# Optimization experiments

Hardware: AMD Instinct MI355X
Metric: run time of the kernel (lower is better)

## Reference

```python
import jax, jax.numpy as jnp
import numpy as np

EPS = 1e-6

def setup_inputs() -> dict:
    key = jax.random.key(0)
    ks = jax.random.split(key, 6)
    N, E, Din, H, D = 50000, 800000, 256, 4, 32
    x = jax.random.normal(ks[0], (N, Din), dtype=jnp.float32)
    adj_indices = jax.random.randint(ks[1], (E, 2), 0, N, dtype=jnp.int32)
    adj_weights = jax.random.uniform(ks[2], (E,), dtype=jnp.float32)
    W = jax.random.normal(ks[3], (Din, H * D), dtype=jnp.float32) * (1.0 / np.sqrt(Din))
    a_src = jax.random.normal(ks[4], (H, D), dtype=jnp.float32)
    a_dst = jax.random.normal(ks[5], (H, D), dtype=jnp.float32)
    return {"x": x, "adj_indices": adj_indices, "adj_weights": adj_weights,
            "W": W, "a_src": a_src, "a_dst": a_dst}

def reference(x, adj_indices, adj_weights, W, a_src, a_dst):
    N = x.shape[0]
    H, D = a_src.shape
    h = (x @ W).reshape(N, H, D)                       # [N,H,D]
    src = adj_indices[:, 0]
    dst = adj_indices[:, 1]
    hs = h[src]                                        # [E,H,D]
    hd = h[dst]                                        # [E,H,D]
    raw = jnp.einsum('ehd,hd->eh', hs, a_src) + jnp.einsum('ehd,hd->eh', hd, a_dst)
    gate = jnp.clip(adj_weights, EPS, None)[:, None]   # [E,1]
    scores = jnp.tanh(raw) + jnp.log(gate)             # [E,H]
    # per-destination segment softmax (numerically stable)
    seg_max = jax.ops.segment_max(scores, dst, num_segments=N)   # [N,H]
    ex = jnp.exp(scores - seg_max[dst])
    denom = jax.ops.segment_sum(ex, dst, num_segments=N)         # [N,H]
    alpha = ex / denom[dst]                            # softmax over edges per dst
    alpha = alpha * gate
    messages = alpha[:, :, None] * hs                  # [E,H,D]
    out = jax.ops.segment_sum(messages, dst, num_segments=N)     # [N,H,D]
    out = out.reshape(N, H * D)
    return jax.nn.gelu(out, approximate=False)
```

## Files before the change

kernel.cpp:

```cpp
#include <hip/hip_runtime.h>
#include <hip/hip_bf16.h>

#define N_NODES 50000
#define N_EDGES 800000
#define DIN 256
#define HD 128
#define NH 4
#define CAP 64
#define CSTR 16

#define GROWS 64
#define LDKH 136

#define GEMM_BLOCKS ((N_NODES + GROWS - 1) / GROWS)
#define SCAT_BLOCKS ((N_EDGES + 255) / 256)

typedef __bf16 bf16x8 __attribute__((ext_vector_type(8)));
typedef float  f32x4  __attribute__((ext_vector_type(4)));

static __device__ __forceinline__ unsigned short f2bu(float v) {
  union { __hip_bfloat16 b; unsigned short u; } c;
  c.b = __float2bfloat16(v);
  return c.u;
}

static __device__ __forceinline__ unsigned short f2hu(float v) {
  union { _Float16 h; unsigned short u; } c;
  c.h = (_Float16)v;
  return c.u;
}

static __device__ __forceinline__ float hu2f(unsigned short u) {
  union { _Float16 h; unsigned short u; } c;
  c.u = u;
  return (float)c.h;
}

__global__ void init_kernel(const float* __restrict__ W,
                            unsigned short* __restrict__ WtF,
                            int* __restrict__ cursor) {
  int i = blockIdx.x * 256 + threadIdx.x;
  if (i < HD * DIN) {
    int j    = i & 7;
    int lane = (i >> 3) & 63;
    int t    = (i >> 9) & 7;
    int s    = (i >> 12) & 3;
    int ks   = (i >> 14) & 1;
    int m = lane & 15, q = lane >> 4;
    int k = ks * 128 + 32 * s + 8 * q + j;
    int c = 16 * t + m;
    WtF[i] = f2bu(W[k * HD + c]);
  }
  if (i < N_NODES * CSTR) cursor[i] = 0;
}

__global__ __launch_bounds__(256, 2) void gemm_kernel(
    const float* __restrict__ x,
    const unsigned short* __restrict__ WtF,
    const float* __restrict__ a_src,
    const float* __restrict__ a_dst,
    unsigned short* __restrict__ hbf,
    float* __restrict__ ssrc,
    float* __restrict__ sdst) {
  __shared__ unsigned short xs[GROWS * LDKH];
  const int tid = threadIdx.x;

  const int row0 = blockIdx.x * GROWS;
  const int wid  = tid >> 6;
  const int lane = tid & 63;
  const int m    = lane & 15;
  const int q    = lane >> 4;

  float4 v0[8];
#pragma unroll
  for (int it = 0; it < 8; it++) {
    int i = it * 256 + tid, r = i >> 5, kq = i & 31;
    int row = row0 + r;
    v0[it] = (row < N_NODES) ? *(const float4*)(x + (size_t)row * DIN + 4 * kq)
                             : make_float4(0.f, 0.f, 0.f, 0.f);
  }
#pragma unroll
  for (int it = 0; it < 8; it++) {
    int i = it * 256 + tid, r = i >> 5, kq = i & 31;
    ushort4 b;
    b.x = f2bu(v0[it].x); b.y = f2bu(v0[it].y); b.z = f2bu(v0[it].z); b.w = f2bu(v0[it].w);
    *(ushort4*)&xs[r * LDKH + 4 * kq] = b;
  }
  __syncthreads();

  f32x4 acc[8];
#pragma unroll
  for (int t = 0; t < 8; t++) acc[t] = (f32x4){0.f, 0.f, 0.f, 0.f};

  const unsigned short* xbase = &xs[(wid * 16 + m) * LDKH];

  bf16x8 a0[4];
#pragma unroll
  for (int s = 0; s < 4; s++) a0[s] = *(const bf16x8*)(xbase + 32 * s + 8 * q);

  float4 v1[8];
#pragma unroll
  for (int it = 0; it < 8; it++) {
    int i = it * 256 + tid, r = i >> 5, kq = i & 31;
    int row = row0 + r;
    v1[it] = (row < N_NODES) ? *(const float4*)(x + (size_t)row * DIN + 128 + 4 * kq)
                             : make_float4(0.f, 0.f, 0.f, 0.f);
  }

#pragma unroll
  for (int s = 0; s < 4; s++) {
    bf16x8 bfr[8];
#pragma unroll
    for (int t = 0; t < 8; t++)
      bfr[t] = *(const bf16x8*)(WtF + (size_t)((0 * 4 + s) * 8 + t) * 512 + lane * 8);
#pragma unroll
    for (int t = 0; t < 8; t++)
      acc[t] = __builtin_amdgcn_mfma_f32_16x16x32_bf16(a0[s], bfr[t], acc[t], 0, 0, 0);
  }
  __syncthreads();

#pragma unroll
  for (int it = 0; it < 8; it++) {
    int i = it * 256 + tid, r = i >> 5, kq = i & 31;
    ushort4 b;
    b.x = f2bu(v1[it].x); b.y = f2bu(v1[it].y); b.z = f2bu(v1[it].z); b.w = f2bu(v1[it].w);
    *(ushort4*)&xs[r * LDKH + 4 * kq] = b;
  }
  __syncthreads();

  bf16x8 a1[4];
#pragma unroll
  for (int s = 0; s < 4; s++) a1[s] = *(const bf16x8*)(xbase + 32 * s + 8 * q);

#pragma unroll
  for (int s = 0; s < 4; s++) {
    bf16x8 bfr[8];
#pragma unroll
    for (int t = 0; t < 8; t++)
      bfr[t] = *(const bf16x8*)(WtF + (size_t)((1 * 4 + s) * 8 + t) * 512 + lane * 8);
#pragma unroll
    for (int t = 0; t < 8; t++)
      acc[t] = __builtin_amdgcn_mfma_f32_16x16x32_bf16(a1[s], bfr[t], acc[t], 0, 0, 0);
  }

#pragma unroll
  for (int t = 0; t < 8; t++) {
#pragma unroll
    for (int r = 0; r < 4; r++) {
      int row = row0 + wid * 16 + q * 4 + r;
      if (row < N_NODES) hbf[(size_t)row * HD + 16 * t + m] = f2bu(acc[t][r]);
    }
  }

  float as[8], ad[8];
#pragma unroll
  for (int t = 0; t < 8; t++) {
    as[t] = a_src[16 * t + m];
    ad[t] = a_dst[16 * t + m];
  }
#pragma unroll
  for (int r = 0; r < 4; r++) {
    float ps[NH] = {0.f, 0.f, 0.f, 0.f};
    float pd[NH] = {0.f, 0.f, 0.f, 0.f};
#pragma unroll
    for (int t = 0; t < 8; t++) {
      ps[t >> 1] = fmaf(acc[t][r], as[t], ps[t >> 1]);
      pd[t >> 1] = fmaf(acc[t][r], ad[t], pd[t >> 1]);
    }
#pragma unroll
    for (int mm = 8; mm >= 1; mm >>= 1) {
#pragma unroll
      for (int hh = 0; hh < NH; hh++) {
        ps[hh] += __shfl_xor(ps[hh], mm, 64);
        pd[hh] += __shfl_xor(pd[hh], mm, 64);
      }
    }
    int row = row0 + wid * 16 + q * 4 + r;
    if (m == 0 && row < N_NODES) {
#pragma unroll
      for (int hh = 0; hh < NH; hh++) {
        ssrc[row * NH + hh] = ps[hh];
        sdst[row * NH + hh] = pd[hh];
      }
    }
  }
}

__global__ __launch_bounds__(256, 4) void scatter_kernel(
    const int2* __restrict__ adj,
    const float* __restrict__ wts,
    int* __restrict__ cursor,
    unsigned int* __restrict__ slots) {
  int e = blockIdx.x * 256 + threadIdx.x;
  if (e >= N_EDGES) return;
  int2 sd = adj[e];
  if ((unsigned)sd.x >= (unsigned)N_NODES || (unsigned)sd.y >= (unsigned)N_NODES) return;
  float g = fmaxf(wts[e], 1e-6f);
  int pos = atomicAdd(&cursor[sd.y * CSTR], 1);
  if (pos >= CAP) pos = CAP - 1;
  unsigned packed = ((unsigned)f2hu(g) << 16) | (unsigned)(sd.x & 0xffff);
  __builtin_nontemporal_store(packed, &slots[((size_t)sd.y << 6) + pos]);
}

__global__ __launch_bounds__(128, 4) void node_kernel(
    const int* __restrict__ cursor,
    const unsigned int* __restrict__ slots,
    const float4* __restrict__ ssrc4,
    const float4* __restrict__ sdst4,
    const unsigned int* __restrict__ hbf32,
    float* __restrict__ out) {
  const int tid  = threadIdx.x;
  const int wid  = tid >> 6;
  const int lane = tid & 63;
  const int n    = blockIdx.x * 2 + wid;
  const int hh   = lane >> 4;

  int deg = cursor[n * CSTR];
  if (deg > CAP) deg = CAP;

  __shared__ int    sidx[2][CAP];
  __shared__ float4 swv[2][CAP];

  float4 ex = make_float4(0.f, 0.f, 0.f, 0.f);
  if (lane < deg) {
    unsigned sl = slots[((size_t)n << 6) + lane];
    int s = (int)(sl & 0xffffu);
    float g = hu2f((unsigned short)(sl >> 16));
    float4 ss = ssrc4[s];
    float4 sd = sdst4[n];
    ex.x = g * expf(tanhf(ss.x + sd.x));
    ex.y = g * expf(tanhf(ss.y + sd.y));
    ex.z = g * expf(tanhf(ss.z + sd.z));
    ex.w = g * expf(tanhf(ss.w + sd.w));
    sidx[wid][lane] = s;
    swv[wid][lane] = make_float4(ex.x * g, ex.y * g, ex.z * g, ex.w * g);
  }

  float4 tot = ex;
#pragma unroll
  for (int mm = 32; mm >= 1; mm >>= 1) {
    tot.x += __shfl_xor(tot.x, mm, 64);
    tot.y += __shfl_xor(tot.y, mm, 64);
    tot.z += __shfl_xor(tot.z, mm, 64);
    tot.w += __shfl_xor(tot.w, mm, 64);
  }
  float dn  = (hh == 0) ? tot.x : (hh == 1) ? tot.y : (hh == 2) ? tot.z : tot.w;
  float inv = (dn > 0.f) ? 1.f / dn : 0.f;
  __syncthreads();

  float acc0 = 0.f, acc1 = 0.f;
  int j = 0;
  for (; j + 8 <= deg; j += 8) {
    int s0 = sidx[wid][j + 0], s1 = sidx[wid][j + 1];
    int s2 = sidx[wid][j + 2], s3 = sidx[wid][j + 3];
    int s4 = sidx[wid][j + 4], s5 = sidx[wid][j + 5];
    int s6 = sidx[wid][j + 6], s7 = sidx[wid][j + 7];
    unsigned u0 = hbf32[(size_t)s0 * (HD / 2) + lane];
    unsigned u1 = hbf32[(size_t)s1 * (HD / 2) + lane];
    unsigned u2 = hbf32[(size_t)s2 * (HD / 2) + lane];
    unsigned u3 = hbf32[(size_t)s3 * (HD / 2) + lane];
    unsigned u4 = hbf32[(size_t)s4 * (HD / 2) + lane];
    unsigned u5 = hbf32[(size_t)s5 * (HD / 2) + lane];
    unsigned u6 = hbf32[(size_t)s6 * (HD / 2) + lane];
    unsigned u7 = hbf32[(size_t)s7 * (HD / 2) + lane];
    float w0 = ((const float*)&swv[wid][j + 0])[hh];
    float w1 = ((const float*)&swv[wid][j + 1])[hh];
    float w2 = ((const float*)&swv[wid][j + 2])[hh];
    float w3 = ((const float*)&swv[wid][j + 3])[hh];
    float w4 = ((const float*)&swv[wid][j + 4])[hh];
    float w5 = ((const float*)&swv[wid][j + 5])[hh];
    float w6 = ((const float*)&swv[wid][j + 6])[hh];
    float w7 = ((const float*)&swv[wid][j + 7])[hh];
    acc0 = fmaf(w0, __uint_as_float(u0 << 16), acc0);
    acc1 = fmaf(w0, __uint_as_float(u0 & 0xffff0000u), acc1);
    acc0 = fmaf(w1, __uint_as_float(u1 << 16), acc0);
    acc1 = fmaf(w1, __uint_as_float(u1 & 0xffff0000u), acc1);
    acc0 = fmaf(w2, __uint_as_float(u2 << 16), acc0);
    acc1 = fmaf(w2, __uint_as_float(u2 & 0xffff0000u), acc1);
    acc0 = fmaf(w3, __uint_as_float(u3 << 16), acc0);
    acc1 = fmaf(w3, __uint_as_float(u3 & 0xffff0000u), acc1);
    acc0 = fmaf(w4, __uint_as_float(u4 << 16), acc0);
    acc1 = fmaf(w4, __uint_as_float(u4 & 0xffff0000u), acc1);
    acc0 = fmaf(w5, __uint_as_float(u5 << 16), acc0);
    acc1 = fmaf(w5, __uint_as_float(u5 & 0xffff0000u), acc1);
    acc0 = fmaf(w6, __uint_as_float(u6 << 16), acc0);
    acc1 = fmaf(w6, __uint_as_float(u6 & 0xffff0000u), acc1);
    acc0 = fmaf(w7, __uint_as_float(u7 << 16), acc0);
    acc1 = fmaf(w7, __uint_as_float(u7 & 0xffff0000u), acc1);
  }
  for (; j < deg; j++) {
    int s0 = sidx[wid][j];
    unsigned u0 = hbf32[(size_t)s0 * (HD / 2) + lane];
    float w0 = ((const float*)&swv[wid][j])[hh];
    acc0 = fmaf(w0, __uint_as_float(u0 << 16), acc0);
    acc1 = fmaf(w0, __uint_as_float(u0 & 0xffff0000u), acc1);
  }
  acc0 *= inv;
  acc1 *= inv;

  float2 gl;
  gl.x = 0.5f * acc0 * (1.f + erff(acc0 * 0.70710678118654752f));
  gl.y = 0.5f * acc1 * (1.f + erff(acc1 * 0.70710678118654752f));
  *(float2*)&out[(size_t)n * HD + 2 * lane] = gl;
}

extern "C" void kernel_launch(void* const* d_in, const int* in_sizes, int n_in,
                              void* d_out, int out_size, void* d_ws, size_t ws_size,
                              hipStream_t stream) {
  const float* x     = (const float*)d_in[0];
  const int2*  adj   = (const int2*)d_in[1];
  const float* wts   = (const float*)d_in[2];
  const float* W     = (const float*)d_in[3];
  const float* a_src = (const float*)d_in[4];
  const float* a_dst = (const float*)d_in[5];
  float* out = (float*)d_out;

  char* p = (char*)d_ws;
  auto carve = [&](size_t bytes) {
    char* q = p;
    p += (bytes + 255) & ~(size_t)255;
    return (void*)q;
  };
  unsigned short* hbf = (unsigned short*)carve((size_t)N_NODES * HD * sizeof(unsigned short));
  unsigned short* WtF = (unsigned short*)carve((size_t)HD * DIN * sizeof(unsigned short));
  float* ssrc   = (float*)carve((size_t)N_NODES * NH * sizeof(float));
  float* sdst   = (float*)carve((size_t)N_NODES * NH * sizeof(float));
  unsigned int* slots = (unsigned int*)carve((size_t)N_NODES * CAP * sizeof(unsigned int));
  int*   cursor = (int*)carve((size_t)N_NODES * CSTR * sizeof(int));

  init_kernel<<<(N_NODES * CSTR + 255) / 256, 256, 0, stream>>>(W, WtF, cursor);
  scatter_kernel<<<SCAT_BLOCKS, 256, 0, stream>>>(adj, wts, cursor, slots);
  gemm_kernel<<<GEMM_BLOCKS, 256, 0, stream>>>(x, WtF, a_src, a_dst, hbf, ssrc, sdst);
  node_kernel<<<N_NODES / 2, 128, 0, stream>>>(cursor, slots, (const float4*)ssrc,
                                               (const float4*)sdst,
                                               (const unsigned int*)hbf, out);
}
```

Measured before the change: 221.3 us.

## Shard per-destination edge buckets by block to reduce atomic contention

Replaces the single padded per-node cursor (stride 16) and 64-slot bucket with 8 shards selected by block index. Each shard has its own dense cursor array and 16-slot buckets. The node kernel gathers the shard counts, compacts the slots into shared memory, and then runs as before. Cursor zeroing moves to hipMemsetAsync so init_kernel only converts W. The change targets atomic contention and the padded cursor footprint, at the cost of more cursor and slot reads per node plus an extra barrier. Per-shard overflow is clamped at 16, whereas the old limit was 64 for the whole node.

```diff
diff --git a/kernel.cpp b/kernel.cpp
--- a/kernel.cpp
+++ b/kernel.cpp
@@ -7,7 +7,8 @@
 #define HD 128
 #define NH 4
 #define CAP 64
-#define CSTR 16
+#define NSH 8
+#define SCAP 16
 
 #define GROWS 64
 #define LDKH 136
@@ -37,8 +38,7 @@
 }
 
 __global__ void init_kernel(const float* __restrict__ W,
-                            unsigned short* __restrict__ WtF,
-                            int* __restrict__ cursor) {
+                            unsigned short* __restrict__ WtF) {
   int i = blockIdx.x * 256 + threadIdx.x;
   if (i < HD * DIN) {
     int j    = i & 7;
@@ -51,7 +51,23 @@
     int c = 16 * t + m;
     WtF[i] = f2bu(W[k * HD + c]);
   }
-  if (i < N_NODES * CSTR) cursor[i] = 0;
+}
+
+__global__ __launch_bounds__(256, 4) void scatter_kernel(
+    const int2* __restrict__ adj,
+    const float* __restrict__ wts,
+    int* __restrict__ cursor_s,
+    unsigned int* __restrict__ slots_s) {
+  int e = blockIdx.x * 256 + threadIdx.x;
+  if (e >= N_EDGES) return;
+  const int shard = blockIdx.x & (NSH - 1);
+  int2 sd = adj[e];
+  if ((unsigned)sd.x >= (unsigned)N_NODES || (unsigned)sd.y >= (unsigned)N_NODES) return;
+  float g = fmaxf(wts[e], 1e-6f);
+  int pos = atomicAdd(&cursor_s[shard * N_NODES + sd.y], 1);
+  if (pos >= SCAP) pos = SCAP - 1;
+  unsigned packed = ((unsigned)f2hu(g) << 16) | (unsigned)(sd.x & 0xffff);
+  slots_s[((size_t)shard * N_NODES + sd.y) * SCAP + pos] = packed;
 }
 
 __global__ __launch_bounds__(256, 2) void gemm_kernel(
@@ -186,25 +202,9 @@
   }
 }
 
-__global__ __launch_bounds__(256, 4) void scatter_kernel(
-    const int2* __restrict__ adj,
-    const float* __restrict__ wts,
-    int* __restrict__ cursor,
-    unsigned int* __restrict__ slots) {
-  int e = blockIdx.x * 256 + threadIdx.x;
-  if (e >= N_EDGES) return;
-  int2 sd = adj[e];
-  if ((unsigned)sd.x >= (unsigned)N_NODES || (unsigned)sd.y >= (unsigned)N_NODES) return;
-  float g = fmaxf(wts[e], 1e-6f);
-  int pos = atomicAdd(&cursor[sd.y * CSTR], 1);
-  if (pos >= CAP) pos = CAP - 1;
-  unsigned packed = ((unsigned)f2hu(g) << 16) | (unsigned)(sd.x & 0xffff);
-  __builtin_nontemporal_store(packed, &slots[((size_t)sd.y << 6) + pos]);
-}
-
 __global__ __launch_bounds__(128, 4) void node_kernel(
-    const int* __restrict__ cursor,
-    const unsigned int* __restrict__ slots,
+    const int* __restrict__ cursor_s,
+    const unsigned int* __restrict__ slots_s,
     const float4* __restrict__ ssrc4,
     const float4* __restrict__ sdst4,
     const unsigned int* __restrict__ hbf32,
@@ -215,15 +215,34 @@
   const int n    = blockIdx.x * 2 + wid;
   const int hh   = lane >> 4;
 
-  int deg = cursor[n * CSTR];
-  if (deg > CAP) deg = CAP;
-
+  __shared__ unsigned spk[2][CAP];
   __shared__ int    sidx[2][CAP];
   __shared__ float4 swv[2][CAP];
 
+  int c[NSH], o[NSH];
+  int tot = 0;
+#pragma unroll
+  for (int s = 0; s < NSH; s++) {
+    int cs = cursor_s[s * N_NODES + n];
+    cs = (cs < SCAP) ? cs : SCAP;
+    c[s] = cs;
+    o[s] = tot;
+    tot += cs;
+  }
+  const int deg = (tot < CAP) ? tot : CAP;
+#pragma unroll
+  for (int s = 0; s < NSH; s++) {
+    if (lane < c[s]) {
+      int d = o[s] + lane;
+      if (d < CAP)
+        spk[wid][d] = slots_s[((size_t)s * N_NODES + n) * SCAP + lane];
+    }
+  }
+  __syncthreads();
+
   float4 ex = make_float4(0.f, 0.f, 0.f, 0.f);
   if (lane < deg) {
-    unsigned sl = slots[((size_t)n << 6) + lane];
+    unsigned sl = spk[wid][lane];
     int s = (int)(sl & 0xffffu);
     float g = hu2f((unsigned short)(sl >> 16));
     float4 ss = ssrc4[s];
@@ -236,15 +255,15 @@
     swv[wid][lane] = make_float4(ex.x * g, ex.y * g, ex.z * g, ex.w * g);
   }
 
-  float4 tot = ex;
+  float4 tot4 = ex;
 #pragma unroll
   for (int mm = 32; mm >= 1; mm >>= 1) {
-    tot.x += __shfl_xor(tot.x, mm, 64);
-    tot.y += __shfl_xor(tot.y, mm, 64);
-    tot.z += __shfl_xor(tot.z, mm, 64);
-    tot.w += __shfl_xor(tot.w, mm, 64);
-  }
-  float dn  = (hh == 0) ? tot.x : (hh == 1) ? tot.y : (hh == 2) ? tot.z : tot.w;
+    tot4.x += __shfl_xor(tot4.x, mm, 64);
+    tot4.y += __shfl_xor(tot4.y, mm, 64);
+    tot4.z += __shfl_xor(tot4.z, mm, 64);
+    tot4.w += __shfl_xor(tot4.w, mm, 64);
+  }
+  float dn  = (hh == 0) ? tot4.x : (hh == 1) ? tot4.y : (hh == 2) ? tot4.z : tot4.w;
   float inv = (dn > 0.f) ? 1.f / dn : 0.f;
   __syncthreads();
 
@@ -325,13 +344,14 @@
   unsigned short* WtF = (unsigned short*)carve((size_t)HD * DIN * sizeof(unsigned short));
   float* ssrc   = (float*)carve((size_t)N_NODES * NH * sizeof(float));
   float* sdst   = (float*)carve((size_t)N_NODES * NH * sizeof(float));
-  unsigned int* slots = (unsigned int*)carve((size_t)N_NODES * CAP * sizeof(unsigned int));
-  int*   cursor = (int*)carve((size_t)N_NODES * CSTR * sizeof(int));
-
-  init_kernel<<<(N_NODES * CSTR + 255) / 256, 256, 0, stream>>>(W, WtF, cursor);
-  scatter_kernel<<<SCAT_BLOCKS, 256, 0, stream>>>(adj, wts, cursor, slots);
+  unsigned int* slots_s = (unsigned int*)carve((size_t)NSH * N_NODES * SCAP * sizeof(unsigned int));
+  int* cursor_s = (int*)carve((size_t)NSH * N_NODES * sizeof(int));
+
+  hipMemsetAsync(cursor_s, 0, (size_t)NSH * N_NODES * sizeof(int), stream);
+  init_kernel<<<(HD * DIN + 255) / 256, 256, 0, stream>>>(W, WtF);
+  scatter_kernel<<<SCAT_BLOCKS, 256, 0, stream>>>(adj, wts, cursor_s, slots_s);
   gemm_kernel<<<GEMM_BLOCKS, 256, 0, stream>>>(x, WtF, a_src, a_dst, hbf, ssrc, sdst);
-  node_kernel<<<N_NODES / 2, 128, 0, stream>>>(cursor, slots, (const float4*)ssrc,
+  node_kernel<<<N_NODES / 2, 128, 0, stream>>>(cursor_s, slots_s, (const float4*)ssrc,
                                                (const float4*)sdst,
                                                (const unsigned int*)hbf, out);
 }
```

Result: slower. 230.4 us (+4.1%).
